# Optimization experiments

Measured on AMD Instinct MI355X. Metric: run time of the kernel, lower is better.

The kernel has to match this reference:

```python
import jax, jax.numpy as jnp
import numpy as np

SIGMA = 1.0   # noise std (unit-variance synthetic input)
P = 11        # patch size p1
K = 16        # number of similar patches k1
WIN = 65      # search window w (odd)
S = 3         # reference-patch stride
ALPHA = 0.5   # n2n alpha


def _unfold(x, ksize, stride):
    # (N,1,H,W) -> (N, ksize*ksize, Ho, Wo); kernel positions row-major (== torch F.unfold for C=1)
    return jax.lax.conv_general_dilated_patches(
        x, (ksize, ksize), (stride, stride), 'VALID',
        dimension_numbers=('NCHW', 'OIHW', 'NCHW'))


def block_matching(x, k, p, w, s):
    N, _, H, W = x.shape
    v = w // 2
    assert (H - p + 1) % s == 1 and (W - p + 1) % s == 1  # no edge-case branches needed
    Href = (H - p) // s + 1
    Wref = (W - p) // s + 1
    x_pad = jnp.pad(x, ((0, 0), (0, 0), (v, v), (v, v)))  # zero pad; invalid candidates masked below
    # |patch|^2 / p^2 at every position of the padded image (== F.avg_pool2d(x**2, p))
    sq = jax.lax.reduce_window(x_pad * x_pad, 0.0, jax.lax.add,
                               (1, 1, p, p), (1, 1, 1, 1), 'VALID') / (p * p)
    norms = _unfold(sq, 2 * v + 1, s)                                  # (N,(2v+1)^2,Href,Wref)
    norms = norms.reshape(N, 2 * v + 1, 2 * v + 1, Href, Wref).transpose(0, 3, 4, 1, 2)
    lw = _unfold(x_pad, 2 * v + p, s) / p                              # (N,(2v+p)^2,Href,Wref)
    lw = lw.reshape(N, 2 * v + p, 2 * v + p, Href, Wref).transpose(0, 3, 4, 1, 2)
    G = N * Href * Wref
    lw = lw.reshape(1, G, 2 * v + p, 2 * v + p)
    ref = lw[0, :, v:-v, v:-v][:, None]                                # (G,1,p,p) reference patches
    sp = jax.lax.conv_general_dilated(
        lw, ref, (1, 1), 'VALID',
        dimension_numbers=('NCHW', 'OIHW', 'NCHW'),
        feature_group_count=G)                                         # (1,G,2v+1,2v+1)
    dist = norms.reshape(1, G, 2 * v + 1, 2 * v + 1) - 2.0 * sp
    dist = dist.reshape(N, Href, Wref, 2 * v + 1, 2 * v + 1)
    # mask candidate patches that fall outside the original image (torch uses NaN padding + topk)
    offs = jnp.arange(-v, v + 1)
    hr = jnp.arange(Href) * s
    wr = jnp.arange(Wref) * s
    row_ok = (hr[:, None] + offs >= 0) & (hr[:, None] + offs <= H - p)  # (Href, 2v+1)
    col_ok = (wr[:, None] + offs >= 0) & (wr[:, None] + offs <= W - p)  # (Wref, 2v+1)
    valid = row_ok[:, None, :, None] & col_ok[None, :, None, :]
    dist = jnp.where(valid[None], dist, jnp.inf)
    dist = dist.at[..., v, v].set(-jnp.inf)                            # reference patch always kept
    dist = dist.reshape(N, Href, Wref, (2 * v + 1) ** 2)
    _, idx = jax.lax.top_k(-dist, k)                                   # k smallest distances
    ind_row = idx // (2 * v + 1) - v
    ind_col = idx % (2 * v + 1) - v
    ind = (ind_row + hr[None, :, None, None]) * (W - p + 1) + (ind_col + wr[None, None, :, None])
    return ind.reshape(N, -1)                                          # (N, Href*Wref*k)


def gather_groups(y, indices, k, p):
    N = y.shape[0]
    uf = _unfold(y, p, 1).reshape(N, p * p, -1)                        # (N, n, (H-p+1)(W-p+1))
    Yg = jnp.take_along_axis(uf, indices[:, None, :], axis=2)          # (N, n, L*k)
    L = indices.shape[1] // k
    return Yg.reshape(N, p * p, L, k).transpose(0, 2, 3, 1)            # (N, L, k, n)


def denoise1(Y, sigma):
    # method='n2n', constraints='affine'
    N, B, k, n = Y.shape
    D = n * sigma ** 2
    E = n * ALPHA ** 2 * sigma ** 2
    Ik = jnp.eye(k, dtype=Y.dtype)
    Q = Y @ jnp.swapaxes(Y, 2, 3) + E * Ik                             # (N,B,k,k), SPD
    Lc = jnp.linalg.cholesky(Q)
    Ikb = jnp.broadcast_to(Ik, Q.shape)
    Z = jax.scipy.linalg.solve_triangular(Lc, Ikb, lower=True)
    Qinv = jax.scipy.linalg.solve_triangular(jnp.swapaxes(Lc, 2, 3), Z, lower=False)
    Qinv1 = jnp.sum(Qinv, axis=3, keepdims=True)
    Qinv2 = jnp.sum(Qinv1, axis=2, keepdims=True)
    theta = Ik - (Qinv - (Qinv1 @ jnp.swapaxes(Qinv1, 2, 3)) / Qinv2) * (D + E)
    theta = jnp.swapaxes(theta, 2, 3)
    X_hat = theta @ Y
    weights = 1.0 / jnp.clip(jnp.sum(theta * theta, axis=3, keepdims=True), 1.0 / k, 1.0)
    return X_hat, weights


def _fold(x, H, W, p):
    # inverse of unfold: sum overlapping p x p patches back onto the image grid
    N, n, _ = x.shape
    Hp, Wp = H - p + 1, W - p + 1
    x = x.reshape(N, p, p, Hp, Wp)
    out = jnp.zeros((N, 1, H, W), x.dtype)
    for a in range(p):
        for b in range(p):
            out = out.at[:, 0, a:a + Hp, b:b + Wp].add(x[:, a, b])
    return out


def aggregate(X_hat, weights, indices, H, W, p):
    N, L, k, n = X_hat.shape
    X = (X_hat * weights).reshape(N, L * k, n).transpose(0, 2, 1)      # (N, n, L*k)
    Wt = jnp.broadcast_to(weights, (N, L, k, n)).reshape(N, L * k, n).transpose(0, 2, 1)
    Lfull = (H - p + 1) * (W - p + 1)
    def scat(vals, idx):
        return jnp.zeros((n, Lfull), vals.dtype).at[:, idx].add(vals)
    X_sum = jax.vmap(scat)(X, indices)
    W_sum = jax.vmap(scat)(Wt, indices)
    return _fold(X_sum, H, W, p) / _fold(W_sum, H, W, p)


def _forward(y):
    N, C, H, W = y.shape
    indices = block_matching(y, K, P, WIN, S)
    Yg = gather_groups(y, indices, K, P)
    X_hat, weights = denoise1(Yg, SIGMA)
    return aggregate(X_hat, weights, indices, H, W, P)


def setup_inputs():
    key = jax.random.key(0)
    y = jax.random.normal(key, (4, 1, 128, 128), dtype=jnp.float32)
    return {"y": y}


def reference(y):
    return _forward(y)
```

## Files before the change

kernel.cpp:

```cpp
#include <hip/hip_runtime.h>
#include <math.h>

#define HH 128
#define WW 128
#define NIMG 4
#define PP 11
#define KSIM 16
#define STRIDE_S 3
#define VRAD 32
#define WINW 65
#define NTASK (WINW*9)
#define HREF 40
#define WREF 40
#define NPOS 118
#define WROWS 75
#define WPITCH 84
#define NGROUP (NIMG*HREF*WREF)
#define EPS_E 30.25f
#define DE_C 151.25f
#define INFD 3.0e38f
#define RTASK (VRAD*9 + VRAD/8)

#define FOOT 84
#define FPITCH 85
#define SPITCH 88

__global__ __launch_bounds__(256, 5)
void bm_kernel(const float* __restrict__ y, int* __restrict__ inds)
{
    __shared__ float win[WROWS][WPITCH];
    __shared__ float swv[4];
    __shared__ int   swi[4];

    const int blk = blockIdx.x;
    const int n   = blk / (HREF*WREF);
    const int rem = blk % (HREF*WREF);
    const int hr  = (rem / WREF) * STRIDE_S;
    const int wr  = (rem % WREF) * STRIDE_S;
    const float* img = y + n * HH * WW;
    const int tid = threadIdx.x;

    for (int t = tid; t < WROWS * WPITCH; t += 256) {
        int r = t / WPITCH, c = t % WPITCH;
        int gr = hr - VRAD + r, gc = wr - VRAD + c;
        float v = 0.f;
        if (c < WROWS && gr >= 0 && gr < HH && gc >= 0 && gc < WW)
            v = img[gr * WW + gc];
        win[r][c] = v;
    }
    __syncthreads();

    float d[3][8];
#pragma unroll
    for (int s = 0; s < 3; s++)
#pragma unroll
        for (int c = 0; c < 8; c++) d[s][c] = INFD;

#pragma unroll
    for (int s = 0; s < 3; s++) {
        int task = tid + (s << 8);
        if (task < NTASK) {
            int drx = task / 9;
            int c0  = (task % 9) * 8;
            int rr  = hr + drx - VRAD;
            bool rowok = (rr >= 0 && rr <= HH - PP);
            if (rowok) {
                float dot[8];
                float colsq[18];
#pragma unroll
                for (int c = 0; c < 8; c++) dot[c] = 0.f;
#pragma unroll
                for (int j2 = 0; j2 < 18; j2++) colsq[j2] = 0.f;
                for (int a = 0; a < PP; a++) {
                    const float4* w4 = reinterpret_cast<const float4*>(&win[drx + a][c0]);
                    float4 A0 = w4[0], A1 = w4[1], A2 = w4[2], A3 = w4[3];
                    float2 A4 = *reinterpret_cast<const float2*>(&win[drx + a][c0 + 16]);
                    float wv[18] = {A0.x,A0.y,A0.z,A0.w, A1.x,A1.y,A1.z,A1.w,
                                    A2.x,A2.y,A2.z,A2.w, A3.x,A3.y,A3.z,A3.w,
                                    A4.x,A4.y};
                    const float4* r4 = reinterpret_cast<const float4*>(&win[VRAD + a][VRAD]);
                    float4 R0 = r4[0], R1 = r4[1];
                    float2 R2 = *reinterpret_cast<const float2*>(&win[VRAD + a][VRAD + 8]);
                    float  R3 = win[VRAD + a][VRAD + 10];
                    float rv[11] = {R0.x,R0.y,R0.z,R0.w, R1.x,R1.y,R1.z,R1.w,
                                    R2.x,R2.y, R3};
#pragma unroll
                    for (int j2 = 0; j2 < 18; j2++) colsq[j2] += wv[j2] * wv[j2];
#pragma unroll
                    for (int b = 0; b < PP; b++) {
#pragma unroll
                        for (int c = 0; c < 8; c++)
                            dot[c] += wv[b + c] * rv[b];
                    }
                }
#pragma unroll
                for (int j2 = 1; j2 < 18; j2++) colsq[j2] += colsq[j2 - 1];
#pragma unroll
                for (int c = 0; c < 8; c++) {
                    int dcx = c0 + c;
                    int cc  = wr + dcx - VRAD;
                    float norm = colsq[c + 10] - (c ? colsq[c - 1] : 0.f);
                    if (dcx < WINW && cc >= 0 && cc <= WW - PP)
                        d[s][c] = norm - 2.f * dot[c];
                }
            }
            if (task == RTASK) d[s][0] = -INFD;
        }
    }

    float lval = INFD; int lidx = 0;
#pragma unroll
    for (int s = 0; s < 3; s++)
#pragma unroll
        for (int c = 0; c < 8; c++)
            if (d[s][c] < lval) { lval = d[s][c]; lidx = (s << 3) | c; }

    for (int sel = 0; sel < KSIM; sel++) {
        float rv = lval;
        int   ri = ((tid + ((lidx >> 3) << 8)) << 3) | (lidx & 7);
#pragma unroll
        for (int off = 32; off > 0; off >>= 1) {
            float ov = __shfl_down(rv, off);
            int   oi = __shfl_down(ri, off);
            if (ov < rv) { rv = ov; ri = oi; }
        }
        if ((tid & 63) == 0) { swv[tid >> 6] = rv; swi[tid >> 6] = ri; }
        __syncthreads();
        float bval = swv[0]; int bidx = swi[0];
#pragma unroll
        for (int w2 = 1; w2 < 4; w2++)
            if (swv[w2] < bval) { bval = swv[w2]; bidx = swi[w2]; }
        if (tid == 0) {
            int task = bidx >> 3;
            int drx = task / 9, dcx = (task % 9) * 8 + (bidx & 7);
            int prr = hr + drx - VRAD, pcc = wr + dcx - VRAD;
            inds[blk * KSIM + sel] = prr * NPOS + pcc;
        }
        __syncthreads();
        int otid = (bidx >> 3) & 255;
        if (tid == otid) {
            int code = (((bidx >> 3) >> 8) << 3) | (bidx & 7);
            lval = INFD; lidx = 0;
#pragma unroll
            for (int s = 0; s < 3; s++)
#pragma unroll
                for (int c = 0; c < 8; c++) {
                    if (((s << 3) | c) == code) d[s][c] = INFD;
                    if (d[s][c] < lval) { lval = d[s][c]; lidx = (s << 3) | c; }
                }
        }
    }
}

__global__ __launch_bounds__(512, 1)
void dn_kernel(const float* __restrict__ y, const int* __restrict__ inds,
               float2* __restrict__ nd, int R)
{
    __shared__ float  src[FOOT][SPITCH];
    __shared__ float2 acc[FOOT][FPITCH];
    __shared__ float  Qm[16][16][17];
    __shared__ float  s1[16][16];
    __shared__ float  s2[16];
    __shared__ float  wl[16][16];
    __shared__ short  pr_[16][16], pc_[16][16];

    const int blk = blockIdx.x;
    const int n  = blk / 100;
    const int tr = blk % 100;
    const int ti = tr / 10, tj = tr % 10;
    const int r0 = 12*ti - VRAD, c0 = 12*tj - VRAD;
    const int tid = threadIdx.x;
    const float* img = y + n * HH * WW;

    if (tid < 256) {
        int g = tid >> 4, m = tid & 15;
        int gg = n*(HREF*WREF) + (ti*4 + (g >> 2))*WREF + (tj*4 + (g & 3));
        int idx = inds[gg*KSIM + m];
        pr_[g][m] = (short)(idx / NPOS);
        pc_[g][m] = (short)(idx % NPOS);
    }
    for (int t = tid; t < FOOT*FOOT; t += 512) {
        int rr = t / FOOT, cc = t % FOOT;
        int gr = r0 + rr, gc = c0 + cc;
        float v = 0.f;
        if (gr >= 0 && gr < HH && gc >= 0 && gc < WW) v = img[gr*WW + gc];
        src[rr][cc] = v;
    }
    for (int t = tid; t < FOOT*FPITCH; t += 512)
        acc[t/FPITCH][t%FPITCH] = make_float2(0.f, 0.f);
    __syncthreads();

    for (int k = 0; k < 5; k++) {
        int task = tid + k*512;
        if (task < 16*136) {
            int g = task / 136, e = task % 136;
            int i = (int)((sqrtf(8.f*(float)e + 1.f) - 1.f) * 0.5f + 1e-4f);
            int j = e - i*(i+1)/2;
            int ari = pr_[g][i] - r0, aci = pc_[g][i] - c0;
            int arj = pr_[g][j] - r0, acj = pc_[g][j] - c0;
            float s = (i == j) ? EPS_E : 0.f;
            for (int a = 0; a < PP; a++) {
                const float* Ri = &src[ari + a][aci];
                const float* Rj = &src[arj + a][acj];
#pragma unroll
                for (int b = 0; b < PP; b++) s += Ri[b] * Rj[b];
            }
            Qm[g][i][j] = s;
            Qm[g][j][i] = s;
        }
    }
    __syncthreads();

    const int uu = tid >> 8, ii = (tid >> 4) & 15, jj = tid & 15;
    for (int ks = 0; ks < 16; ks++) {
        float fA[8], rk[8], pv[8], aij[8];
#pragma unroll
        for (int k = 0; k < 8; k++) {
            int g = uu + 2*k;
            fA[k]  = Qm[g][ii][ks];
            rk[k]  = Qm[g][ks][jj];
            pv[k]  = Qm[g][ks][ks];
            aij[k] = Qm[g][ii][jj];
        }
        __syncthreads();
#pragma unroll
        for (int k = 0; k < 8; k++) {
            int g = uu + 2*k;
            float inv = 1.f / pv[k];
            float nv;
            if (ii == ks) nv = (jj == ks) ? inv : rk[k] * inv;
            else          nv = (jj == ks) ? -fA[k] * inv : aij[k] - fA[k] * rk[k] * inv;
            Qm[g][ii][jj] = nv;
        }
        __syncthreads();
    }

    if (tid < 256) {
        int g = tid >> 4, a = tid & 15;
        float s = 0.f;
#pragma unroll
        for (int b = 0; b < 16; b++) s += Qm[g][a][b];
        s1[g][a] = s;
    }
    __syncthreads();
    if (tid < 16) {
        float s = 0.f;
#pragma unroll
        for (int a = 0; a < 16; a++) s += s1[tid][a];
        s2[tid] = s;
    }
    __syncthreads();
#pragma unroll
    for (int k = 0; k < 8; k++) {
        int g = uu + 2*k;
        float t = ((ii == jj) ? 1.f : 0.f)
                - (Qm[g][ii][jj] - s1[g][ii]*s1[g][jj]/s2[g]) * DE_C;
        Qm[g][ii][jj] = t;
    }
    __syncthreads();
    if (tid < 256) {
        int g = tid >> 4, r = tid & 15;
        float s = 0.f;
#pragma unroll
        for (int m2 = 0; m2 < 16; m2++) { float t = Qm[g][m2][r]; s += t*t; }
        s = fminf(fmaxf(s, 1.f/16.f), 1.f);
        wl[g][r] = 1.f / s;
    }
    __syncthreads();

    {
        const int g6 = tid >> 5, q6 = tid & 31;
        const int pxb = q6 * 4;
        int drp[4], dcp[4]; bool okp[4];
#pragma unroll
        for (int p = 0; p < 4; p++) {
            int px = pxb + p;
            okp[p] = (px < 121);
            int pxc = okp[p] ? px : 0;
            drp[p] = pxc / 11; dcp[p] = pxc % 11;
        }
        float xh[16][4];
#pragma unroll
        for (int r = 0; r < 16; r++)
#pragma unroll
            for (int p = 0; p < 4; p++) xh[r][p] = 0.f;
#pragma unroll
        for (int m2 = 0; m2 < 16; m2++) {
            int ar = pr_[g6][m2] - r0, ac = pc_[g6][m2] - c0;
            float tv[16];
#pragma unroll
            for (int r = 0; r < 16; r++) tv[r] = Qm[g6][m2][r];
            float yv[4];
#pragma unroll
            for (int p = 0; p < 4; p++) yv[p] = src[ar + drp[p]][ac + dcp[p]];
#pragma unroll
            for (int r = 0; r < 16; r++)
#pragma unroll
                for (int p = 0; p < 4; p++) xh[r][p] += tv[r] * yv[p];
        }
#pragma unroll
        for (int r = 0; r < 16; r++) {
            int ar = pr_[g6][r] - r0, ac = pc_[g6][r] - c0;
            float wv2 = wl[g6][r];
#pragma unroll
            for (int p = 0; p < 4; p++) {
                if (okp[p]) {
                    float* cell = (float*)&acc[ar + drp[p]][ac + dcp[p]];
                    __hip_atomic_fetch_add(cell,     wv2 * xh[r][p],
                        __ATOMIC_RELAXED, __HIP_MEMORY_SCOPE_WORKGROUP);
                    __hip_atomic_fetch_add(cell + 1, wv2,
                        __ATOMIC_RELAXED, __HIP_MEMORY_SCOPE_WORKGROUP);
                }
            }
        }
    }
    __syncthreads();

    float2* ndI = nd + ((size_t)(blk & (R - 1)) * NIMG + n) * HH * WW;
    for (int t = tid; t < FOOT * FOOT; t += 512) {
        int rr = t / FOOT, cc = t % FOOT;
        float2 v = acc[rr][cc];
        if (v.y != 0.f) {
            int px = (r0 + rr) * WW + (c0 + cc);
#if defined(__has_builtin) && __has_builtin(__builtin_amdgcn_global_atomic_fadd_v2f32)
            typedef float v2f __attribute__((ext_vector_type(2)));
            __builtin_amdgcn_global_atomic_fadd_v2f32((v2f*)&ndI[px], (v2f){v.x, v.y});
#else
            atomicAdd(&ndI[px].x, v.x);
            atomicAdd(&ndI[px].y, v.y);
#endif
        }
    }
}

__global__ __launch_bounds__(256)
void fin_kernel(const float2* __restrict__ nd, float* __restrict__ out, int R)
{
    int t = blockIdx.x * 256 + threadIdx.x;
    if (t < NIMG * HH * WW) {
        float sn = 0.f, sd = 0.f;
        for (int r = 0; r < R; r++) {
            float2 v = nd[(size_t)r * NIMG * HH * WW + t];
            sn += v.x; sd += v.y;
        }
        out[t] = sn / sd;
    }
}

extern "C" void kernel_launch(void* const* d_in, const int* in_sizes, int n_in,
                              void* d_out, int out_size, void* d_ws, size_t ws_size,
                              hipStream_t stream)
{
    const float* y = (const float*)d_in[0];
    float* out = (float*)d_out;

    size_t indsBytes = (size_t)NGROUP * KSIM * sizeof(int);
    size_t perRep    = (size_t)NIMG * HH * WW * sizeof(float2);
    int R = 1;
    while (R < 4 && indsBytes + perRep * (size_t)(R * 2) <= ws_size) R <<= 1;

    float2* nd  = (float2*)d_ws;
    int*    inds = (int*)((char*)d_ws + perRep * (size_t)R);

    hipMemsetAsync(nd, 0, perRep * (size_t)R, stream);
    bm_kernel<<<NGROUP, 256, 0, stream>>>(y, inds);
    dn_kernel<<<NIMG * 100, 512, 0, stream>>>(y, inds, nd, R);
    fin_kernel<<<(NIMG * HH * WW + 255) / 256, 256, 0, stream>>>(nd, out, R);
}
```

Baseline: 492.3 us.

## Use per-wave top-k selection with final merge; rebalance denoise reconstruction work

In block matching, each wave now finds its own 16 best candidates without block-wide barriers per selection step. A single wave then merges the 4x16 candidates into the final top-16. This removes two __syncthreads per selection iteration. The denoise reconstruction loop is remapped so each thread handles one group and two pixels, giving 976 tasks over two passes instead of the 4-pixel tiling, which cuts wasted padded pixels and register pressure. The cost is an extra serial merge phase in one wave and some threads idle in the second pass.

```diff
diff --git a/kernel.cpp b/kernel.cpp
--- a/kernel.cpp
+++ b/kernel.cpp
@@ -29,8 +29,8 @@
 void bm_kernel(const float* __restrict__ y, int* __restrict__ inds)
 {
     __shared__ float win[WROWS][WPITCH];
-    __shared__ float swv[4];
-    __shared__ int   swi[4];
+    __shared__ float candv[4][16];
+    __shared__ int   candi[4][16];
 
     const int blk = blockIdx.x;
     const int n   = blk / (HREF*WREF);
@@ -115,6 +115,7 @@
         for (int c = 0; c < 8; c++)
             if (d[s][c] < lval) { lval = d[s][c]; lidx = (s << 3) | c; }
 
+    const int wvid = tid >> 6, lane = tid & 63;
     for (int sel = 0; sel < KSIM; sel++) {
         float rv = lval;
         int   ri = ((tid + ((lidx >> 3) << 8)) << 3) | (lidx & 7);
@@ -124,22 +125,11 @@
             int   oi = __shfl_down(ri, off);
             if (ov < rv) { rv = ov; ri = oi; }
         }
-        if ((tid & 63) == 0) { swv[tid >> 6] = rv; swi[tid >> 6] = ri; }
-        __syncthreads();
-        float bval = swv[0]; int bidx = swi[0];
-#pragma unroll
-        for (int w2 = 1; w2 < 4; w2++)
-            if (swv[w2] < bval) { bval = swv[w2]; bidx = swi[w2]; }
-        if (tid == 0) {
-            int task = bidx >> 3;
-            int drx = task / 9, dcx = (task % 9) * 8 + (bidx & 7);
-            int prr = hr + drx - VRAD, pcc = wr + dcx - VRAD;
-            inds[blk * KSIM + sel] = prr * NPOS + pcc;
-        }
-        __syncthreads();
-        int otid = (bidx >> 3) & 255;
+        if (lane == 0) { candv[wvid][sel] = rv; candi[wvid][sel] = ri; }
+        int bi = __shfl(ri, 0);
+        int otid = (bi >> 3) & 255;
         if (tid == otid) {
-            int code = (((bidx >> 3) >> 8) << 3) | (bidx & 7);
+            int code = (((bi >> 3) >> 8) << 3) | (bi & 7);
             lval = INFD; lidx = 0;
 #pragma unroll
             for (int s = 0; s < 3; s++)
@@ -148,6 +138,31 @@
                     if (((s << 3) | c) == code) d[s][c] = INFD;
                     if (d[s][c] < lval) { lval = d[s][c]; lidx = (s << 3) | c; }
                 }
+        }
+    }
+    __syncthreads();
+
+    if (wvid == 0) {
+        float v  = candv[lane >> 4][lane & 15];
+        int   ci = candi[lane >> 4][lane & 15];
+        for (int sel = 0; sel < KSIM; sel++) {
+            float rv = v; int ri = ci; int rl = lane;
+#pragma unroll
+            for (int off = 32; off > 0; off >>= 1) {
+                float ov = __shfl_down(rv, off);
+                int   oi = __shfl_down(ri, off);
+                int   ol = __shfl_down(rl, off);
+                if (ov < rv) { rv = ov; ri = oi; rl = ol; }
+            }
+            int bi = __shfl(ri, 0);
+            int bl = __shfl(rl, 0);
+            if (lane == 0) {
+                int task2 = bi >> 3;
+                int drx = task2 / 9, dcx = (task2 % 9) * 8 + (bi & 7);
+                inds[blk * KSIM + sel] =
+                    (hr + drx - VRAD) * NPOS + (wr + dcx - VRAD);
+            }
+            if (lane == bl) v = INFD;
         }
     }
 }
@@ -268,47 +283,52 @@
     }
     __syncthreads();
 
-    {
-        const int g6 = tid >> 5, q6 = tid & 31;
-        const int pxb = q6 * 4;
-        int drp[4], dcp[4]; bool okp[4];
-#pragma unroll
-        for (int p = 0; p < 4; p++) {
-            int px = pxb + p;
-            okp[p] = (px < 121);
-            int pxc = okp[p] ? px : 0;
-            drp[p] = pxc / 11; dcp[p] = pxc % 11;
-        }
-        float xh[16][4];
-#pragma unroll
-        for (int r = 0; r < 16; r++)
-#pragma unroll
-            for (int p = 0; p < 4; p++) xh[r][p] = 0.f;
-#pragma unroll
-        for (int m2 = 0; m2 < 16; m2++) {
-            int ar = pr_[g6][m2] - r0, ac = pc_[g6][m2] - c0;
-            float tv[16];
-#pragma unroll
-            for (int r = 0; r < 16; r++) tv[r] = Qm[g6][m2][r];
-            float yv[4];
-#pragma unroll
-            for (int p = 0; p < 4; p++) yv[p] = src[ar + drp[p]][ac + dcp[p]];
-#pragma unroll
-            for (int r = 0; r < 16; r++)
-#pragma unroll
-                for (int p = 0; p < 4; p++) xh[r][p] += tv[r] * yv[p];
-        }
-#pragma unroll
-        for (int r = 0; r < 16; r++) {
-            int ar = pr_[g6][r] - r0, ac = pc_[g6][r] - c0;
-            float wv2 = wl[g6][r];
-#pragma unroll
-            for (int p = 0; p < 4; p++) {
-                if (okp[p]) {
-                    float* cell = (float*)&acc[ar + drp[p]][ac + dcp[p]];
-                    __hip_atomic_fetch_add(cell,     wv2 * xh[r][p],
+    for (int it = 0; it < 2; it++) {
+        int task = tid + it*512;
+        if (task < 16*61) {
+            int g = task / 61, s = task % 61;
+            int pxa = 2*s;
+            bool okB = (pxa + 1 < 121);
+            int dra = pxa / 11, dca = pxa % 11;
+            int drb = dra, dcb = dca + 1;
+            if (dcb == 11) { drb = dra + 1; dcb = 0; }
+            if (!okB) { drb = dra; dcb = dca; }
+
+            int baseS[16];
+#pragma unroll
+            for (int m = 0; m < 16; m++)
+                baseS[m] = ((int)pr_[g][m] - r0) * SPITCH + ((int)pc_[g][m] - c0);
+
+            const float* sf = &src[0][0];
+            float xhA[16], xhB[16];
+#pragma unroll
+            for (int r = 0; r < 16; r++) { xhA[r] = 0.f; xhB[r] = 0.f; }
+            const int offA = dra*SPITCH + dca, offB = drb*SPITCH + dcb;
+#pragma unroll
+            for (int m = 0; m < 16; m++) {
+                float yvA = sf[baseS[m] + offA];
+                float yvB = sf[baseS[m] + offB];
+#pragma unroll
+                for (int r = 0; r < 16; r++) {
+                    float t = Qm[g][m][r];
+                    xhA[r] += t * yvA;
+                    xhB[r] += t * yvB;
+                }
+            }
+#pragma unroll
+            for (int r = 0; r < 16; r++) {
+                float wv2 = wl[g][r];
+                int ar = (int)pr_[g][r] - r0, ac = (int)pc_[g][r] - c0;
+                float* cA = (float*)&acc[ar + dra][ac + dca];
+                __hip_atomic_fetch_add(cA,     wv2 * xhA[r],
+                    __ATOMIC_RELAXED, __HIP_MEMORY_SCOPE_WORKGROUP);
+                __hip_atomic_fetch_add(cA + 1, wv2,
+                    __ATOMIC_RELAXED, __HIP_MEMORY_SCOPE_WORKGROUP);
+                if (okB) {
+                    float* cB = (float*)&acc[ar + drb][ac + dcb];
+                    __hip_atomic_fetch_add(cB,     wv2 * xhB[r],
                         __ATOMIC_RELAXED, __HIP_MEMORY_SCOPE_WORKGROUP);
-                    __hip_atomic_fetch_add(cell + 1, wv2,
+                    __hip_atomic_fetch_add(cB + 1, wv2,
                         __ATOMIC_RELAXED, __HIP_MEMORY_SCOPE_WORKGROUP);
                 }
             }
```

After: 504.3 us. 1.02x slower.

## Halve denoise accumulator LDS via two-pass row halves and remap BM task order

Applied to the files above, without the earlier changes.

The denoise kernel's shared float2 accumulator is cut to half height and filled in two passes over the 84 rows, each followed by a flush to global memory. The per-thread 16x4 register tile of estimates is replaced by a one-pixel-per-thread formulation, with the weights pre-folded into Qm. The block-matching kernel now orders tasks row-offset-fastest instead of column-chunk-fastest, which changes shared-memory access patterns and the tie-breaking order. The LDS saving may allow more resident blocks, but the patch estimates are recomputed in each half, adding arithmetic and extra barriers.

```diff
diff --git a/kernel.cpp b/kernel.cpp
--- a/kernel.cpp
+++ b/kernel.cpp
@@ -19,7 +19,7 @@
 #define EPS_E 30.25f
 #define DE_C 151.25f
 #define INFD 3.0e38f
-#define RTASK (VRAD*9 + VRAD/8)
+#define RTASK 292
 
 #define FOOT 84
 #define FPITCH 85
@@ -60,8 +60,8 @@
     for (int s = 0; s < 3; s++) {
         int task = tid + (s << 8);
         if (task < NTASK) {
-            int drx = task / 9;
-            int c0  = (task % 9) * 8;
+            int drx = task % WINW;
+            int c0  = (task / WINW) * 8;
             int rr  = hr + drx - VRAD;
             bool rowok = (rr >= 0 && rr <= HH - PP);
             if (rowok) {
@@ -131,10 +131,11 @@
         for (int w2 = 1; w2 < 4; w2++)
             if (swv[w2] < bval) { bval = swv[w2]; bidx = swi[w2]; }
         if (tid == 0) {
-            int task = bidx >> 3;
-            int drx = task / 9, dcx = (task % 9) * 8 + (bidx & 7);
-            int prr = hr + drx - VRAD, pcc = wr + dcx - VRAD;
-            inds[blk * KSIM + sel] = prr * NPOS + pcc;
+            int task2 = bidx >> 3;
+            int drx = task2 % WINW;
+            int dcx = (task2 / WINW) * 8 + (bidx & 7);
+            inds[blk * KSIM + sel] =
+                (hr + drx - VRAD) * NPOS + (wr + dcx - VRAD);
         }
         __syncthreads();
         int otid = (bidx >> 3) & 255;
@@ -157,7 +158,7 @@
                float2* __restrict__ nd, int R)
 {
     __shared__ float  src[FOOT][SPITCH];
-    __shared__ float2 acc[FOOT][FPITCH];
+    __shared__ float2 accH[42][FPITCH];
     __shared__ float  Qm[16][16][17];
     __shared__ float  s1[16][16];
     __shared__ float  s2[16];
@@ -168,34 +169,32 @@
     const int n  = blk / 100;
     const int tr = blk % 100;
     const int ti = tr / 10, tj = tr % 10;
-    const int r0 = 12*ti - VRAD, c0 = 12*tj - VRAD;
+    const int r0 = 12 * ti - VRAD, c0 = 12 * tj - VRAD;
     const int tid = threadIdx.x;
     const float* img = y + n * HH * WW;
 
     if (tid < 256) {
         int g = tid >> 4, m = tid & 15;
-        int gg = n*(HREF*WREF) + (ti*4 + (g >> 2))*WREF + (tj*4 + (g & 3));
-        int idx = inds[gg*KSIM + m];
+        int gg = n * (HREF * WREF) + (ti * 4 + (g >> 2)) * WREF + (tj * 4 + (g & 3));
+        int idx = inds[gg * KSIM + m];
         pr_[g][m] = (short)(idx / NPOS);
         pc_[g][m] = (short)(idx % NPOS);
     }
-    for (int t = tid; t < FOOT*FOOT; t += 512) {
+    for (int t = tid; t < FOOT * FOOT; t += 512) {
         int rr = t / FOOT, cc = t % FOOT;
         int gr = r0 + rr, gc = c0 + cc;
-        float v = 0.f;
-        if (gr >= 0 && gr < HH && gc >= 0 && gc < WW) v = img[gr*WW + gc];
-        src[rr][cc] = v;
-    }
-    for (int t = tid; t < FOOT*FPITCH; t += 512)
-        acc[t/FPITCH][t%FPITCH] = make_float2(0.f, 0.f);
+        float vv = 0.f;
+        if (gr >= 0 && gr < HH && gc >= 0 && gc < WW) vv = img[gr * WW + gc];
+        src[rr][cc] = vv;
+    }
     __syncthreads();
 
     for (int k = 0; k < 5; k++) {
-        int task = tid + k*512;
-        if (task < 16*136) {
+        int task = tid + k * 512;
+        if (task < 16 * 136) {
             int g = task / 136, e = task % 136;
-            int i = (int)((sqrtf(8.f*(float)e + 1.f) - 1.f) * 0.5f + 1e-4f);
-            int j = e - i*(i+1)/2;
+            int i = (int)((sqrtf(8.f * (float)e + 1.f) - 1.f) * 0.5f + 1e-4f);
+            int j = e - i * (i + 1) / 2;
             int ari = pr_[g][i] - r0, aci = pc_[g][i] - c0;
             int arj = pr_[g][j] - r0, acj = pc_[g][j] - c0;
             float s = (i == j) ? EPS_E : 0.f;
@@ -216,7 +215,7 @@
         float fA[8], rk[8], pv[8], aij[8];
 #pragma unroll
         for (int k = 0; k < 8; k++) {
-            int g = uu + 2*k;
+            int g = uu + 2 * k;
             fA[k]  = Qm[g][ii][ks];
             rk[k]  = Qm[g][ks][jj];
             pv[k]  = Qm[g][ks][ks];
@@ -225,7 +224,7 @@
         __syncthreads();
 #pragma unroll
         for (int k = 0; k < 8; k++) {
-            int g = uu + 2*k;
+            int g = uu + 2 * k;
             float inv = 1.f / pv[k];
             float nv;
             if (ii == ks) nv = (jj == ks) ? inv : rk[k] * inv;
@@ -239,7 +238,7 @@
         int g = tid >> 4, a = tid & 15;
         float s = 0.f;
 #pragma unroll
-        for (int b = 0; b < 16; b++) s += Qm[g][a][b];
+        for (int b2 = 0; b2 < 16; b2++) s += Qm[g][a][b2];
         s1[g][a] = s;
     }
     __syncthreads();
@@ -252,9 +251,9 @@
     __syncthreads();
 #pragma unroll
     for (int k = 0; k < 8; k++) {
-        int g = uu + 2*k;
+        int g = uu + 2 * k;
         float t = ((ii == jj) ? 1.f : 0.f)
-                - (Qm[g][ii][jj] - s1[g][ii]*s1[g][jj]/s2[g]) * DE_C;
+                - (Qm[g][ii][jj] - s1[g][ii] * s1[g][jj] / s2[g]) * DE_C;
         Qm[g][ii][jj] = t;
     }
     __syncthreads();
@@ -262,74 +261,71 @@
         int g = tid >> 4, r = tid & 15;
         float s = 0.f;
 #pragma unroll
-        for (int m2 = 0; m2 < 16; m2++) { float t = Qm[g][m2][r]; s += t*t; }
-        s = fminf(fmaxf(s, 1.f/16.f), 1.f);
+        for (int m2 = 0; m2 < 16; m2++) { float t = Qm[g][m2][r]; s += t * t; }
+        s = fminf(fmaxf(s, 1.f / 16.f), 1.f);
         wl[g][r] = 1.f / s;
     }
     __syncthreads();
-
-    {
-        const int g6 = tid >> 5, q6 = tid & 31;
-        const int pxb = q6 * 4;
-        int drp[4], dcp[4]; bool okp[4];
-#pragma unroll
-        for (int p = 0; p < 4; p++) {
-            int px = pxb + p;
-            okp[p] = (px < 121);
-            int pxc = okp[p] ? px : 0;
-            drp[p] = pxc / 11; dcp[p] = pxc % 11;
-        }
-        float xh[16][4];
-#pragma unroll
-        for (int r = 0; r < 16; r++)
-#pragma unroll
-            for (int p = 0; p < 4; p++) xh[r][p] = 0.f;
-#pragma unroll
-        for (int m2 = 0; m2 < 16; m2++) {
-            int ar = pr_[g6][m2] - r0, ac = pc_[g6][m2] - c0;
-            float tv[16];
-#pragma unroll
-            for (int r = 0; r < 16; r++) tv[r] = Qm[g6][m2][r];
-            float yv[4];
-#pragma unroll
-            for (int p = 0; p < 4; p++) yv[p] = src[ar + drp[p]][ac + dcp[p]];
-#pragma unroll
-            for (int r = 0; r < 16; r++)
-#pragma unroll
-                for (int p = 0; p < 4; p++) xh[r][p] += tv[r] * yv[p];
-        }
-#pragma unroll
-        for (int r = 0; r < 16; r++) {
-            int ar = pr_[g6][r] - r0, ac = pc_[g6][r] - c0;
-            float wv2 = wl[g6][r];
-#pragma unroll
-            for (int p = 0; p < 4; p++) {
-                if (okp[p]) {
-                    float* cell = (float*)&acc[ar + drp[p]][ac + dcp[p]];
-                    __hip_atomic_fetch_add(cell,     wv2 * xh[r][p],
-                        __ATOMIC_RELAXED, __HIP_MEMORY_SCOPE_WORKGROUP);
-                    __hip_atomic_fetch_add(cell + 1, wv2,
-                        __ATOMIC_RELAXED, __HIP_MEMORY_SCOPE_WORKGROUP);
+#pragma unroll
+    for (int k = 0; k < 8; k++) {
+        int g = uu + 2 * k;
+        Qm[g][ii][jj] *= wl[g][jj];
+    }
+    __syncthreads();
+
+    float2* ndI = nd + ((size_t)(blk & (R - 1)) * NIMG + n) * HH * WW;
+#pragma unroll 1
+    for (int half = 0; half < 2; half++) {
+        const int h0 = half * 42;
+        for (int t = tid; t < 42 * FPITCH; t += 512)
+            ((float2*)accH)[t] = make_float2(0.f, 0.f);
+        __syncthreads();
+
+        for (int it = 0; it < 4; it++) {
+            int task = tid + it * 512;
+            if (task < 16 * 121) {
+                int g = task / 121, px = task % 121;
+                int dra = px / 11, dca = px % 11;
+                float yv[16];
+#pragma unroll
+                for (int m = 0; m < 16; m++)
+                    yv[m] = src[(int)pr_[g][m] - r0 + dra][(int)pc_[g][m] - c0 + dca];
+#pragma unroll
+                for (int r = 0; r < 16; r++) {
+                    int ar = (int)pr_[g][r] - r0;
+                    int hA = ar + dra;
+                    if (hA >= h0 && hA < h0 + 42) {
+                        float xw = 0.f;
+#pragma unroll
+                        for (int m = 0; m < 16; m++)
+                            xw += Qm[g][m][r] * yv[m];
+                        int ac = (int)pc_[g][r] - c0;
+                        float* cell = (float*)&accH[hA - h0][ac + dca];
+                        __hip_atomic_fetch_add(cell,     xw,
+                            __ATOMIC_RELAXED, __HIP_MEMORY_SCOPE_WORKGROUP);
+                        __hip_atomic_fetch_add(cell + 1, wl[g][r],
+                            __ATOMIC_RELAXED, __HIP_MEMORY_SCOPE_WORKGROUP);
+                    }
                 }
             }
         }
-    }
-    __syncthreads();
-
-    float2* ndI = nd + ((size_t)(blk & (R - 1)) * NIMG + n) * HH * WW;
-    for (int t = tid; t < FOOT * FOOT; t += 512) {
-        int rr = t / FOOT, cc = t % FOOT;
-        float2 v = acc[rr][cc];
-        if (v.y != 0.f) {
-            int px = (r0 + rr) * WW + (c0 + cc);
+        __syncthreads();
+
+        for (int t = tid; t < 42 * FOOT; t += 512) {
+            int rr = t / FOOT, cc = t % FOOT;
+            float2 vv = accH[rr][cc];
+            if (vv.y != 0.f) {
+                int px = (r0 + h0 + rr) * WW + (c0 + cc);
 #if defined(__has_builtin) && __has_builtin(__builtin_amdgcn_global_atomic_fadd_v2f32)
-            typedef float v2f __attribute__((ext_vector_type(2)));
-            __builtin_amdgcn_global_atomic_fadd_v2f32((v2f*)&ndI[px], (v2f){v.x, v.y});
+                typedef float v2f __attribute__((ext_vector_type(2)));
+                __builtin_amdgcn_global_atomic_fadd_v2f32((v2f*)&ndI[px], (v2f){vv.x, vv.y});
 #else
-            atomicAdd(&ndI[px].x, v.x);
-            atomicAdd(&ndI[px].y, v.y);
+                atomicAdd(&ndI[px].x, vv.x);
+                atomicAdd(&ndI[px].y, vv.y);
 #endif
-        }
+            }
+        }
+        __syncthreads();
     }
 }
 
@@ -340,8 +336,8 @@
     if (t < NIMG * HH * WW) {
         float sn = 0.f, sd = 0.f;
         for (int r = 0; r < R; r++) {
-            float2 v = nd[(size_t)r * NIMG * HH * WW + t];
-            sn += v.x; sd += v.y;
+            float2 vv = nd[(size_t)r * NIMG * HH * WW + t];
+            sn += vv.x; sd += vv.y;
         }
         out[t] = sn / sd;
     }
@@ -354,12 +350,12 @@
     const float* y = (const float*)d_in[0];
     float* out = (float*)d_out;
 
-    size_t indsBytes = (size_t)NGROUP * KSIM * sizeof(int);
-    size_t perRep    = (size_t)NIMG * HH * WW * sizeof(float2);
+    size_t perRep = (size_t)NIMG * HH * WW * sizeof(float2);
+    size_t indsB  = (size_t)NGROUP * KSIM * sizeof(int);
     int R = 1;
-    while (R < 4 && indsBytes + perRep * (size_t)(R * 2) <= ws_size) R <<= 1;
-
-    float2* nd  = (float2*)d_ws;
+    while (R < 4 && perRep * (size_t)(R * 2) + indsB <= ws_size) R <<= 1;
+
+    float2* nd   = (float2*)d_ws;
     int*    inds = (int*)((char*)d_ws + perRep * (size_t)R);
 
     hipMemsetAsync(nd, 0, perRep * (size_t)R, stream);
```

New measurement: 446.6 us. -9.3%, faster.
